# Kernel tuning notes

Measured on AMD Instinct MI355X. Metric: run time of the kernel, lower is better.

## Reference

```python
import jax, jax.numpy as jnp
from jax import lax
import numpy as np

B, C, HS, WS = 64, 1024, 23, 23  # backbone features (stride-16 of a 368x368 crop)
K = 28  # keypoints


def setup_inputs() -> dict:
    key = jax.random.key(0)
    ks = jax.random.split(key, 20)
    w = lambda k, shape, s=0.05: jax.random.normal(k, shape, jnp.float32) * s
    inp = {}
    inp["x"] = jax.random.normal(ks[0], (B, C, HS, WS), jnp.float32)
    # Residual(1024, 1024) block res5a (conv4 skipped: numIn == numOut, resConv False)
    inp["r5a_w1"] = w(ks[1], (512, 1024, 1, 1)); inp["r5a_b1"] = jnp.zeros(512, jnp.float32)
    inp["r5a_g1"] = jnp.ones(512, jnp.float32); inp["r5a_be1"] = jnp.zeros(512, jnp.float32)
    inp["r5a_m1"] = w(ks[2], (512,), 0.1)
    inp["r5a_v1"] = jax.random.uniform(ks[3], (512,), jnp.float32, 0.5, 1.5)
    inp["r5a_w2"] = w(ks[4], (512, 512, 3, 3)); inp["r5a_b2"] = jnp.zeros(512, jnp.float32)
    inp["r5a_g2"] = jnp.ones(512, jnp.float32); inp["r5a_be2"] = jnp.zeros(512, jnp.float32)
    inp["r5a_m2"] = w(ks[5], (512,), 0.1)
    inp["r5a_v2"] = jax.random.uniform(ks[6], (512,), jnp.float32, 0.5, 1.5)
    inp["r5a_w3"] = w(ks[7], (1024, 512, 1, 1)); inp["r5a_b3"] = jnp.zeros(1024, jnp.float32)
    # res5b 1x1 -> 3x3 -> 1x1
    inp["b1_w"] = w(ks[8], (256, 1024, 1, 1)); inp["b1_b"] = jnp.zeros(256, jnp.float32)
    inp["b2_w"] = w(ks[9], (128, 256, 3, 3)); inp["b2_b"] = jnp.zeros(128, jnp.float32)
    inp["b3_w"] = w(ks[10], (256, 128, 1, 1)); inp["b3_b"] = jnp.zeros(256, jnp.float32)
    # ConvTranspose2d weights kept in torch layout (Cin, Cout, kH, kW)
    inp["c1_w"] = w(ks[11], (256, 63, 4, 4)); inp["c1_b"] = jnp.zeros(63, jnp.float32)
    inp["c2_w"] = w(ks[12], (256, 128, 4, 4)); inp["c2_b"] = jnp.zeros(128, jnp.float32)
    # head convs
    inp["f1_w"] = w(ks[13], (128, 212, 3, 3)); inp["f1_b"] = jnp.zeros(128, jnp.float32)
    inp["f2_w"] = w(ks[14], (112, 128, 1, 1)); inp["f2_b"] = jnp.zeros(112, jnp.float32)
    return inp


_DN = ("NCHW", "OIHW", "NCHW")


def _conv(t, w, b, pad=0):
    y = lax.conv_general_dilated(t, w, (1, 1), [(pad, pad), (pad, pad)], dimension_numbers=_DN)
    return y + b[None, :, None, None]


def _deconv(t, w, b):
    # torch ConvTranspose2d(k=4, s=2, p=1): flip spatial, swap I/O, use lhs dilation
    wt = jnp.flip(w, (2, 3)).transpose(1, 0, 2, 3)  # (Cout, Cin, 4, 4)
    y = lax.conv_general_dilated(t, wt, (1, 1), [(2, 2), (2, 2)], lhs_dilation=(2, 2),
                                 dimension_numbers=_DN)
    return y + b[None, :, None, None]


def _bn(t, g, be, m, v):
    scale = g * lax.rsqrt(v + 1e-5)
    return (t - m[None, :, None, None]) * scale[None, :, None, None] + be[None, :, None, None]


def reference(x, r5a_w1, r5a_b1, r5a_g1, r5a_be1, r5a_m1, r5a_v1,
              r5a_w2, r5a_b2, r5a_g2, r5a_be2, r5a_m2, r5a_v2,
              r5a_w3, r5a_b3, b1_w, b1_b, b2_w, b2_b, b3_w, b3_b,
              c1_w, c1_b, c2_w, c2_b, f1_w, f1_b, f2_w, f2_b):
    # res5a: Residual(1024, 1024) -- identity shortcut (conv4 branch not taken)
    h = jax.nn.relu(_bn(_conv(x, r5a_w1, r5a_b1), r5a_g1, r5a_be1, r5a_m1, r5a_v1))
    h = jax.nn.relu(_bn(_conv(h, r5a_w2, r5a_b2, pad=1), r5a_g2, r5a_be2, r5a_m2, r5a_v2))
    h = _conv(h, r5a_w3, r5a_b3) + x
    # res5b
    h = _conv(h, b1_w, b1_b)
    h = _conv(h, b2_w, b2_b, pad=1)
    h = _conv(h, b3_w, b3_b)
    out1 = _deconv(h, c1_w, c1_b)              # [B, 63, 2H, 2W] location maps
    out2 = jax.nn.relu(_deconv(h, c2_w, c2_b))  # [B, 128, 2H, 2W]
    # per-keypoint location-map magnitude: sqrt(x^2 + y^2 + z^2) over interleaved channels
    out3 = jnp.sqrt(out1[:, ::3] ** 2 + out1[:, 1::3] ** 2 + out1[:, 2::3] ** 2)  # [B, 21, ...]
    cat = jnp.concatenate([out1, out2, out3], axis=1)  # 63 + 128 + 21 = 212 channels
    h = jax.nn.relu(_conv(cat, f1_w, f1_b, pad=1))
    h = _conv(h, f2_w, f2_b)                   # [B, 112, Hh, Wh]
    Bn, _, Hh, Wh = h.shape
    o = h.reshape(Bn, 4, Wh, Hh, K)            # faithful to torch .view(B, 4, W, H, 28)
    heatmap, map_x, map_y, map_z = o[:, 0], o[:, 1], o[:, 2], o[:, 3]
    hm_val = heatmap.max(axis=1)               # [B, Hh, K]
    hm_idx = heatmap.argmax(axis=1)            # [B, Hh, K]
    hm_idx2 = hm_val.argmax(axis=1)            # [B, K]
    hm_idx1 = jnp.take_along_axis(hm_idx, hm_idx2[:, None, :], axis=1)[:, 0]  # [B, K]
    bi = jnp.arange(Bn)[:, None]
    ki = jnp.arange(K)[None, :]
    vx = map_x[bi, hm_idx1, hm_idx2, ki]       # vectorized form of the nested python loop
    vy = map_y[bi, hm_idx1, hm_idx2, ki]
    vz = map_z[bi, hm_idx1, hm_idx2, ki]
    out_mod = jnp.stack([vx, vy, vz], axis=-1).reshape(Bn, 3 * K)  # [B, 84]
    return out_mod
```

## Files before the change

kernel.cpp:

```cpp
#include <hip/hip_runtime.h>
#include <math.h>

typedef __attribute__((ext_vector_type(8))) _Float16 f16x8;
typedef __attribute__((ext_vector_type(4))) float f32x4;

union HU { _Float16 h; unsigned short u; };

__device__ __forceinline__ void split32(float v, unsigned short& hh, unsigned short& ll) {
    HU a, b;
    a.h = (_Float16)v;
    b.h = (_Float16)(v - (float)a.h);
    hh = a.u; ll = b.u;
}
__device__ __forceinline__ float h2f(unsigned short s) { HU a; a.u = s; return (float)a.h; }

__device__ __forceinline__ void gload16(const unsigned short* g, unsigned short* l) {
    __builtin_amdgcn_global_load_lds(
        (const __attribute__((address_space(1))) unsigned int*)g,
        (__attribute__((address_space(3))) unsigned int*)l, 16, 0, 0);
}

struct ConvP {
    const unsigned short* in;
    const unsigned short* wr;
    const float* bias;
    const float* resx;
    unsigned short* out;
    long long loIn, loW, loOut;
    int H, W;
    int inWP, inPix0, inImg;
    int CIp, T, wRow, pxTotal;
    int oImg, oPix0, oYstr, oXstr, oC, oChOff, CO;
    int resCstr, resImg, relu;
    int shift[16];
    int woff[16];
};

template<int NFRAG>
__global__ __launch_bounds__(256) void convmm(ConvP p)
{
    __shared__ unsigned short lAh[128 * 32];
    __shared__ unsigned short lAl[128 * 32];
    __shared__ unsigned short lBh[128 * 32];
    __shared__ unsigned short lBl[128 * 32];

    const int tid  = threadIdx.x;
    const int w    = tid >> 6;
    const int lane = tid & 63;
    const int lo   = lane & 15, hi = lane >> 4;
    const int wm   = w >> 1,    wn = w & 1;
    const int HW   = p.H * p.W;

    long long aOff[2];
    const int aoct = lane & 3;
    for (int j = 0; j < 2; ++j) {
        int instr = 2 * w + j;
        int px = blockIdx.x * 128 + instr * 16 + (lane >> 2);
        if (px >= p.pxTotal) px = p.pxTotal - 1;
        int n = px / HW, pr = px - n * HW;
        int y = pr / p.W, x = pr - y * p.W;
        aOff[j] = ((long long)n * p.inImg + p.inPix0 + y * p.inWP + x) * (long long)p.CIp
                  + aoct * 8;
    }
    constexpr int NB = NFRAG / 2;
    long long bOff[NB];
    const int cob = blockIdx.y * (NFRAG * 32);
    for (int j = 0; j < NB; ++j) {
        int instr = NB * w + j;
        int col = instr * 16 + (lane >> 2);
        bOff[j] = (long long)(cob + col) * p.wRow + aoct * 8;
    }

    f32x4 acc[4][NFRAG];
#pragma unroll
    for (int q = 0; q < 4; ++q)
#pragma unroll
        for (int r = 0; r < NFRAG; ++r) acc[q][r] = (f32x4){0.f, 0.f, 0.f, 0.f};

    for (int t = 0; t < p.T; ++t) {
        const long long tShift = (long long)p.shift[t] * p.CIp;
        const int wo = p.woff[t];
        for (int ci0 = 0; ci0 < p.CIp; ci0 += 32) {
            __syncthreads();
#pragma unroll
            for (int j = 0; j < 2; ++j) {
                gload16(p.in + aOff[j] + tShift + ci0,          &lAh[(2 * w + j) * 512]);
                gload16(p.in + p.loIn + aOff[j] + tShift + ci0, &lAl[(2 * w + j) * 512]);
            }
#pragma unroll
            for (int j = 0; j < NB; ++j) {
                gload16(p.wr + bOff[j] + wo + ci0,         &lBh[(NB * w + j) * 512]);
                gload16(p.wr + p.loW + bOff[j] + wo + ci0, &lBl[(NB * w + j) * 512]);
            }
            __syncthreads();

            f16x8 aFh[4], aFl[4], bFh[NFRAG], bFl[NFRAG];
#pragma unroll
            for (int q = 0; q < 4; ++q) {
                int idx = (wm * 64 + q * 16 + lo) * 32 + hi * 8;
                aFh[q] = *(const f16x8*)&lAh[idx];
                aFl[q] = *(const f16x8*)&lAl[idx];
            }
#pragma unroll
            for (int r = 0; r < NFRAG; ++r) {
                int idx = (wn * NFRAG * 16 + r * 16 + lo) * 32 + hi * 8;
                bFh[r] = *(const f16x8*)&lBh[idx];
                bFl[r] = *(const f16x8*)&lBl[idx];
            }
#pragma unroll
            for (int q = 0; q < 4; ++q)
#pragma unroll
                for (int r = 0; r < NFRAG; ++r)
                    acc[q][r] = __builtin_amdgcn_mfma_f32_16x16x32_f16(
                        aFh[q], bFh[r], acc[q][r], 0, 0, 0);
#pragma unroll
            for (int q = 0; q < 4; ++q)
#pragma unroll
                for (int r = 0; r < NFRAG; ++r)
                    acc[q][r] = __builtin_amdgcn_mfma_f32_16x16x32_f16(
                        aFh[q], bFl[r], acc[q][r], 0, 0, 0);
#pragma unroll
            for (int q = 0; q < 4; ++q)
#pragma unroll
                for (int r = 0; r < NFRAG; ++r)
                    acc[q][r] = __builtin_amdgcn_mfma_f32_16x16x32_f16(
                        aFl[q], bFh[r], acc[q][r], 0, 0, 0);
        }
    }

    const int coB = cob + wn * NFRAG * 16;
#pragma unroll
    for (int q = 0; q < 4; ++q) {
        int pxBase = blockIdx.x * 128 + wm * 64 + q * 16 + hi * 4;
#pragma unroll
        for (int r4 = 0; r4 < 4; ++r4) {
            int px = pxBase + r4;
            if (px >= p.pxTotal) continue;
            int n = px / HW, pr = px - n * HW;
            int y = pr / p.W, x = pr - y * p.W;
            long long obase = ((long long)n * p.oImg + p.oPix0 + y * p.oYstr + x * p.oXstr)
                              * (long long)p.oC + p.oChOff;
#pragma unroll
            for (int nf = 0; nf < NFRAG; ++nf) {
                int co = coB + nf * 16 + lo;
                if (co < p.CO) {
                    float v = acc[q][nf][r4] + p.bias[co];
                    if (p.resx)
                        v += p.resx[(long long)n * p.resImg + (long long)co * p.resCstr + pr];
                    if (p.relu) v = fmaxf(v, 0.f);
                    unsigned short vh, vl;
                    split32(v, vh, vl);
                    p.out[obase + co] = vh;
                    p.out[p.loOut + obase + co] = vl;
                }
            }
        }
    }
}

__global__ __launch_bounds__(256) void prep_x(const float* __restrict__ in,
                                              unsigned short* __restrict__ xp,
                                              long long loOff)
{
    __shared__ float t[64][65];
    const int n = blockIdx.z, c0 = blockIdx.y * 64, px0 = blockIdx.x * 64;
    const int tid = threadIdx.x;
    const int colA = tid & 63, rowA = tid >> 6;
#pragma unroll
    for (int i = 0; i < 16; ++i) {
        int cl = i * 4 + rowA;
        int px = px0 + colA;
        float v = 0.f;
        if (px < 529) v = in[((size_t)n * 1024 + c0 + cl) * 529 + px];
        t[cl][colA] = v;
    }
    __syncthreads();
#pragma unroll
    for (int i = 0; i < 16; ++i) {
        int pxl = i * 4 + rowA;
        int px = px0 + pxl;
        if (px < 529) {
            unsigned short vh, vl;
            split32(t[colA][pxl], vh, vl);
            long long o = ((long long)n * 529 + px) * 1024 + c0 + colA;
            xp[o] = vh; xp[o + loOff] = vl;
        }
    }
}

__global__ __launch_bounds__(256) void prep_w(const float* __restrict__ src,
                                              unsigned short* __restrict__ dst, long long loW,
                                              int CO, int CI, int T, int COp, int CIp,
                                              const float* __restrict__ scale)
{
    long long idx = (long long)blockIdx.x * 256 + threadIdx.x;
    long long tot = (long long)COp * T * CIp;
    if (idx >= tot) return;
    int ci = idx % CIp; long long r = idx / CIp;
    int t = r % T; int co = r / T;
    float v = 0.f;
    if (co < CO && ci < CI) {
        v = src[((long long)co * CI + ci) * T + t];
        if (scale) v *= scale[co];
    }
    unsigned short vh, vl;
    split32(v, vh, vl);
    dst[idx] = vh; dst[idx + loW] = vl;
}

__global__ __launch_bounds__(256) void prep_w_deconv(const float* __restrict__ src,
                                                     unsigned short* __restrict__ dst,
                                                     long long loW, int CO)
{
    int idx = blockIdx.x * 256 + threadIdx.x;
    if (idx >= 128 * 16 * 256) return;
    int ci = idx & 255; int r = idx >> 8;
    int tap = r & 15; int co = r >> 4;
    int ky = tap >> 2, kx = tap & 3;
    float v = 0.f;
    if (co < CO) v = src[((size_t)ci * CO + co) * 16 + (3 - ky) * 4 + (3 - kx)];
    unsigned short vh, vl;
    split32(v, vh, vl);
    dst[idx] = vh; dst[idx + loW] = vl;
}

__global__ __launch_bounds__(512) void prep_sb(
    const float* g1, const float* be1, const float* m1, const float* v1, const float* b1,
    const float* g2, const float* be2, const float* m2, const float* v2, const float* b2,
    float* s1, float* bb1, float* s2, float* bb2)
{
    int i = threadIdx.x;
    float s = g1[i] * rsqrtf(v1[i] + 1e-5f);
    s1[i] = s; bb1[i] = (b1[i] - m1[i]) * s + be1[i];
    s = g2[i] * rsqrtf(v2[i] + 1e-5f);
    s2[i] = s; bb2[i] = (b2[i] - m2[i]) * s + be2[i];
}

__global__ __launch_bounds__(256) void zero_border(unsigned short* buf,
                                                   int HP, int WP, int C, int nb)
{
    long long idx = (long long)blockIdx.x * 256 + threadIdx.x;
    long long tot = (long long)64 * nb * C;
    if (idx >= tot) return;
    int c = idx % C; long long r = idx / C;
    int b = r % nb; int n = r / nb;
    int pp;
    if (b < WP) pp = b;
    else if (b < 2 * WP) pp = (HP - 1) * WP + (b - WP);
    else { int q = b - 2 * WP; int row = 1 + (q >> 1); pp = row * WP + ((q & 1) ? (WP - 1) : 0); }
    buf[((long long)n * HP * WP + pp) * C + c] = 0;
}

__global__ __launch_bounds__(256) void zero_chpad(unsigned short* cat)
{
    long long idx = (long long)blockIdx.x * 256 + threadIdx.x;
    if (idx >= (long long)64 * 2304 * 12) return;
    int c = 212 + (int)(idx % 12);
    long long pp = idx / 12;
    cat[pp * 224 + c] = 0;
}

__global__ __launch_bounds__(256) void out3_k(unsigned short* cat, long long loOff)
{
    long long idx = (long long)blockIdx.x * 256 + threadIdx.x;
    if (idx >= (long long)64 * 2116 * 21) return;
    int j = idx % 21; long long r = idx / 21;
    int pr = r % 2116; int n = r / 2116;
    int y = pr / 46, x = pr - y * 46;
    long long base = ((long long)n * 2304 + (y + 1) * 48 + (x + 1)) * 224;
    float a = h2f(cat[base + 3 * j])     + h2f(cat[base + 3 * j + loOff]);
    float b = h2f(cat[base + 3 * j + 1]) + h2f(cat[base + 3 * j + 1 + loOff]);
    float c = h2f(cat[base + 3 * j + 2]) + h2f(cat[base + 3 * j + 2 + loOff]);
    unsigned short vh, vl;
    split32(sqrtf(a * a + b * b + c * c), vh, vl);
    cat[base + 191 + j] = vh;
    cat[base + 191 + j + loOff] = vl;
}

__global__ __launch_bounds__(64) void argmax_hl(const unsigned short* __restrict__ h,
                                                long long loOff, float* __restrict__ outp)
{
    const int k = blockIdx.x, n = blockIdx.y, t = threadIdx.x;
    const unsigned short* b = h + (size_t)n * 2116 * 112;
    float best = -INFINITY; int ba = 0; int bb = t;
    if (t < 46) {
        for (int a = 0; a < 46; ++a) {
            int f = a * 1288 + t * 28 + k;
            int c = f / 2116, pr = f - c * 2116;
            long long e = (long long)pr * 112 + c;
            float v = h2f(b[e]) + h2f(b[e + loOff]);
            if (v > best) { best = v; ba = a; }
        }
    }
#pragma unroll
    for (int off = 32; off > 0; off >>= 1) {
        float ov = __shfl_down(best, off);
        int oa = __shfl_down(ba, off), ob = __shfl_down(bb, off);
        if (ov > best || (ov == best && ob < bb)) { best = ov; ba = oa; bb = ob; }
    }
    if (t == 0) {
        for (int q = 1; q <= 3; ++q) {
            int f = q * 59248 + ba * 1288 + bb * 28 + k;
            int c = f / 2116, pr = f - c * 2116;
            long long e = (long long)pr * 112 + c;
            outp[(size_t)n * 84 + k * 3 + (q - 1)] = h2f(b[e]) + h2f(b[e + loOff]);
        }
    }
}

extern "C" void kernel_launch(void* const* d_in, const int* in_sizes, int n_in,
                              void* d_out, int out_size, void* d_ws, size_t ws_size,
                              hipStream_t stream)
{
    const float* x   = (const float*)d_in[0];
    const float* w1  = (const float*)d_in[1];
    const float* rb1 = (const float*)d_in[2];
    const float* g1  = (const float*)d_in[3];
    const float* be1 = (const float*)d_in[4];
    const float* m1  = (const float*)d_in[5];
    const float* v1  = (const float*)d_in[6];
    const float* w2  = (const float*)d_in[7];
    const float* rb2 = (const float*)d_in[8];
    const float* g2  = (const float*)d_in[9];
    const float* be2 = (const float*)d_in[10];
    const float* m2  = (const float*)d_in[11];
    const float* v2  = (const float*)d_in[12];
    const float* w3  = (const float*)d_in[13];
    const float* rb3 = (const float*)d_in[14];
    const float* b1w = (const float*)d_in[15];
    const float* b1b = (const float*)d_in[16];
    const float* b2w = (const float*)d_in[17];
    const float* b2b = (const float*)d_in[18];
    const float* b3w = (const float*)d_in[19];
    const float* b3b = (const float*)d_in[20];
    const float* c1w = (const float*)d_in[21];
    const float* c1b = (const float*)d_in[22];
    const float* c2w = (const float*)d_in[23];
    const float* c2b = (const float*)d_in[24];
    const float* f1w = (const float*)d_in[25];
    const float* f1b = (const float*)d_in[26];
    const float* f2w = (const float*)d_in[27];
    const float* f2b = (const float*)d_in[28];

    unsigned short* wsb = (unsigned short*)d_ws;
    size_t woffE = 0;
    auto walloc = [&](size_t planeElems) {
        unsigned short* p = wsb + woffE; woffE += 2 * planeElems; return p;
    };
    unsigned short* Wr1  = walloc(524288);
    unsigned short* Wr2  = walloc(2359296);
    unsigned short* Wr3  = walloc(524288);
    unsigned short* Wr4  = walloc(262144);
    unsigned short* Wr5  = walloc(294912);
    unsigned short* Wr6  = walloc(32768);
    unsigned short* Wr7  = walloc(524288);
    unsigned short* Wr8  = walloc(524288);
    unsigned short* Wr9  = walloc(258048);
    unsigned short* Wr10 = walloc(16384);
    char* fscr = (char*)d_ws + 23068672;
    float* s1  = (float*)(fscr);
    float* bb1 = (float*)(fscr + 2048);
    float* s2  = (float*)(fscr + 4096);
    float* bb2 = (float*)(fscr + 6144);

    unsigned short* XPU = wsb + 12582912;
    unsigned short* R1  = wsb + 81920000;
    unsigned short* R2  = wsb + 12582912;
    unsigned short* R3  = wsb + 47251456;
    unsigned short* B1  = wsb + 116588544;
    unsigned short* B2  = wsb + 12582912;
    unsigned short* B3  = wsb + 21250048;
    unsigned short* CAT = wsb + 47251456;
    unsigned short* F1  = wsb + 12582912;
    unsigned short* F2  = wsb + 47251456;
    const long long XPU_L = 34668544, R1_L = 20480000, R2_L = 17334272, R3_L = 34668544;
    const long long B1_L = 10240000, B2_L = 4333568, B3_L = 10240000;
    const long long CAT_L = 33030144, F1_L = 17334272, F2_L = 15167488;

    prep_sb<<<1, 512, 0, stream>>>(g1, be1, m1, v1, rb1, g2, be2, m2, v2, rb2, s1, bb1, s2, bb2);
    auto pw = [&](const float* src, unsigned short* dst, long long loW, int CO, int CI,
                  int T, int COp, int CIp, const float* sc) {
        long long tot = (long long)COp * T * CIp;
        prep_w<<<(tot + 255) / 256, 256, 0, stream>>>(src, dst, loW, CO, CI, T, COp, CIp, sc);
    };
    pw(w1,  Wr1, 524288,  512, 1024, 1, 512, 1024, s1);
    pw(w2,  Wr2, 2359296, 512, 512,  9, 512, 512,  s2);
    pw(w3,  Wr3, 524288,  1024, 512, 1, 1024, 512, nullptr);
    pw(b1w, Wr4, 262144,  256, 1024, 1, 256, 1024, nullptr);
    pw(b2w, Wr5, 294912,  128, 256,  9, 128, 256,  nullptr);
    pw(b3w, Wr6, 32768,   256, 128,  1, 256, 128,  nullptr);
    prep_w_deconv<<<(128 * 16 * 256) / 256, 256, 0, stream>>>(c1w, Wr7, 524288, 63);
    prep_w_deconv<<<(128 * 16 * 256) / 256, 256, 0, stream>>>(c2w, Wr8, 524288, 128);
    pw(f1w, Wr9, 258048,  128, 212,  9, 128, 224,  nullptr);
    pw(f2w, Wr10, 16384,  112, 128,  1, 128, 128,  nullptr);
    prep_x<<<dim3(9, 16, 64), 256, 0, stream>>>(x, XPU, XPU_L);

    auto zb = [&](unsigned short* buf, long long loOff, int HP, int WP, int C) {
        int nb = 2 * WP + 2 * (HP - 2);
        long long tot = (long long)64 * nb * C;
        zero_border<<<(tot + 255) / 256, 256, 0, stream>>>(buf, HP, WP, C, nb);
        zero_border<<<(tot + 255) / 256, 256, 0, stream>>>(buf + loOff, HP, WP, C, nb);
    };

    auto conv = [&](int NFRAG, const unsigned short* in, long long loIn,
                    const unsigned short* wr, long long loW,
                    const float* bias, const float* resx, unsigned short* outp, long long loOut,
                    int H, int W, int inWP, int inPix0, int inImg, int CIp, int T, int wRow,
                    int oImg, int oPix0, int oYstr, int oXstr, int oC, int oChOff, int CO,
                    int relu, const int* shifts, const int* woffs) {
        ConvP p{};
        p.in = in; p.wr = wr; p.bias = bias; p.resx = resx; p.out = outp;
        p.loIn = loIn; p.loW = loW; p.loOut = loOut;
        p.H = H; p.W = W; p.inWP = inWP; p.inPix0 = inPix0; p.inImg = inImg;
        p.CIp = CIp; p.T = T; p.wRow = wRow; p.pxTotal = 64 * H * W;
        p.oImg = oImg; p.oPix0 = oPix0; p.oYstr = oYstr; p.oXstr = oXstr;
        p.oC = oC; p.oChOff = oChOff; p.CO = CO;
        p.resCstr = 529; p.resImg = 541696; p.relu = relu;
        for (int t = 0; t < T; ++t) { p.shift[t] = shifts[t]; p.woff[t] = woffs[t]; }
        int BN = NFRAG * 32;
        dim3 grid((p.pxTotal + 127) / 128, (CO + BN - 1) / BN);
        if (NFRAG == 4) convmm<4><<<grid, 256, 0, stream>>>(p);
        else            convmm<2><<<grid, 256, 0, stream>>>(p);
    };

    int z16[16] = {0};
    int sh9_25[16], wo9_512[16], wo9_256[16], sh9_48[16], wo9_224[16];
    for (int t = 0; t < 9; ++t) {
        int ky = t / 3, kx = t % 3;
        sh9_25[t] = (ky - 1) * 25 + (kx - 1);
        sh9_48[t] = (ky - 1) * 48 + (kx - 1);
        wo9_512[t] = t * 512; wo9_256[t] = t * 256; wo9_224[t] = t * 224;
    }

    zb(R1, R1_L, 25, 25, 512);
    conv(4, XPU, XPU_L, Wr1, 524288, bb1, nullptr, R1, R1_L,
         23, 23, 23, 0, 529, 1024, 1, 1024, 625, 26, 25, 1, 512, 0, 512, 1, z16, z16);
    conv(4, R1, R1_L, Wr2, 2359296, bb2, nullptr, R2, R2_L,
         23, 23, 25, 26, 625, 512, 9, 9 * 512, 529, 0, 23, 1, 512, 0, 512, 1, sh9_25, wo9_512);
    zb(B1, B1_L, 25, 25, 256);
    conv(4, R2, R2_L, Wr3, 524288, rb3, x, R3, R3_L,
         23, 23, 23, 0, 529, 512, 1, 512, 529, 0, 23, 1, 1024, 0, 1024, 0, z16, z16);
    zb(B3, B3_L, 25, 25, 256);
    conv(4, R3, R3_L, Wr4, 262144, b1b, nullptr, B1, B1_L,
         23, 23, 23, 0, 529, 1024, 1, 1024, 625, 26, 25, 1, 256, 0, 256, 0, z16, z16);
    zb(CAT, CAT_L, 48, 48, 224);
    {
        long long tot = (long long)64 * 2304 * 12;
        zero_chpad<<<(tot + 255) / 256, 256, 0, stream>>>(CAT);
        zero_chpad<<<(tot + 255) / 256, 256, 0, stream>>>(CAT + CAT_L);
    }
    conv(4, B1, B1_L, Wr5, 294912, b2b, nullptr, B2, B2_L,
         23, 23, 25, 26, 625, 256, 9, 9 * 256, 529, 0, 23, 1, 128, 0, 128, 0, sh9_25, wo9_256);
    conv(4, B2, B2_L, Wr6, 32768, b3b, nullptr, B3, B3_L,
         23, 23, 23, 0, 529, 128, 1, 128, 625, 26, 25, 1, 256, 0, 256, 0, z16, z16);

    for (int a = 0; a < 2; ++a)
        for (int b = 0; b < 2; ++b) {
            int sh[16], wo[16];
            for (int ty = 0; ty < 2; ++ty)
                for (int tx = 0; tx < 2; ++tx) {
                    int tI = ty * 2 + tx;
                    sh[tI] = (a + ty - 1) * 25 + (b + tx - 1);
                    wo[tI] = ((a + 2 * ty) * 4 + (b + 2 * tx)) * 256;
                }
            int oPix0 = (a + 1) * 48 + (b + 1);
            conv(2, B3, B3_L, Wr7, 524288, c1b, nullptr, CAT, CAT_L,
                 23, 23, 25, 26, 625, 256, 4, 16 * 256, 2304, oPix0, 96, 2, 224, 0, 63,
                 0, sh, wo);
            conv(4, B3, B3_L, Wr8, 524288, c2b, nullptr, CAT, CAT_L,
                 23, 23, 25, 26, 625, 256, 4, 16 * 256, 2304, oPix0, 96, 2, 224, 63, 128,
                 1, sh, wo);
        }
    {
        long long tot = (long long)64 * 2116 * 21;
        out3_k<<<(tot + 255) / 256, 256, 0, stream>>>(CAT, CAT_L);
    }

    conv(4, CAT, CAT_L, Wr9, 258048, f1b, nullptr, F1, F1_L,
         46, 46, 48, 49, 2304, 224, 9, 9 * 224, 2116, 0, 46, 1, 128, 0, 128, 1,
         sh9_48, wo9_224);
    conv(2, F1, F1_L, Wr10, 16384, f2b, nullptr, F2, F2_L,
         46, 46, 46, 0, 2116, 128, 1, 128, 2116, 0, 46, 1, 112, 0, 112, 0, z16, z16);

    argmax_hl<<<dim3(28, 64), dim3(64), 0, stream>>>(F2, F2_L, (float*)d_out);
}
```

Baseline: 2.559 ms.

## Stage halo input tile once per channel chunk for spatial convolutions

Adds a convhalo kernel that loads a contiguous input window, covering the 128-pixel block plus its halo, into LDS once per 32-channel chunk. All taps then read from it through shifted offsets, and only the weight tiles are double-buffered per tap. The goal is to stop re-fetching the input tile for every one of the 9 (or 4) taps, cutting global and LDS traffic for the 3x3 convs and the deconv phases. It also remaps workgroups across the 8 XCDs so neighbouring blocks share cache, and it groups images into units. In exchange it uses a larger LDS footprint and adds a sync per tap, and the halo indexing must stay within the padded buffers.

```diff
diff --git a/kernel.cpp b/kernel.cpp
--- a/kernel.cpp
+++ b/kernel.cpp
@@ -147,6 +147,169 @@
                     float v = acc[q][nf][r4] + p.bias[co];
                     if (p.resx)
                         v += p.resx[(long long)n * p.resImg + (long long)co * p.resCstr + pr];
+                    if (p.relu) v = fmaxf(v, 0.f);
+                    unsigned short vh, vl;
+                    split32(v, vh, vl);
+                    p.out[obase + co] = vh;
+                    p.out[p.loOut + obase + co] = vl;
+                }
+            }
+        }
+    }
+}
+
+struct HConvP {
+    const unsigned short* in;
+    const unsigned short* wr;
+    const float* bias;
+    unsigned short* out;
+    long long loIn, loW, loOut;
+    int W, IMG_PX, UNIT, UNIT_PX, BPI, nUnits;
+    int inWP, inPix0, inImg, halo;
+    int CIp, T, wRow;
+    int oImg, oPix0, oYstr, oXstr, oC, oChOff, CO;
+    int relu;
+    int shift[16];
+    int woff[16];
+};
+
+template<int NFRAG>
+__global__ __launch_bounds__(256) void convhalo(HConvP p)
+{
+    __shared__ unsigned short sA[2 * 8192];
+    __shared__ unsigned short sB[2][8192];
+
+    const int tid  = threadIdx.x;
+    const int w    = tid >> 6;
+    const int lane = tid & 63;
+    const int lo   = lane & 15, hi = lane >> 4;
+    const int hi8  = hi * 8;
+    const int wm   = w >> 1,    wn = w & 1;
+
+    const int nwg = gridDim.x, orig = blockIdx.x;
+    const int q8 = nwg >> 3, r8 = nwg & 7;
+    const int xcd = orig & 7, lcl = orig >> 3;
+    const int l = (xcd < r8 ? xcd * (q8 + 1) : r8 * (q8 + 1) + (xcd - r8) * q8) + lcl;
+    const int upb = p.nUnits * p.BPI;
+    const int co_blk = l / upb;
+    const int rest = l - co_blk * upb;
+    const int unit = rest / p.BPI;
+    const int b = rest - unit * p.BPI;
+    const int cob = co_blk * (NFRAG * 32);
+
+    const int px0 = b * 128;
+    const int n0 = unit * p.UNIT + px0 / p.IMG_PX;
+    const int pr0 = px0 % p.IMG_PX;
+    const long long stageBase = (long long)n0 * p.inImg + p.inPix0
+                                + (pr0 / p.W) * p.inWP + (pr0 % p.W) - p.halo;
+
+    int lpx[4];
+#pragma unroll
+    for (int q = 0; q < 4; ++q) {
+        int pl = px0 + wm * 64 + q * 16 + lo;
+        if (pl >= p.UNIT_PX) pl = p.UNIT_PX - 1;
+        int nn = unit * p.UNIT + pl / p.IMG_PX;
+        int pr = pl % p.IMG_PX;
+        long long pp = (long long)nn * p.inImg + p.inPix0
+                       + (pr / p.W) * p.inWP + (pr % p.W);
+        lpx[q] = (int)(pp - stageBase);
+    }
+
+    const unsigned short* srcA = p.in + (stageBase + (lane >> 2)) * (long long)p.CIp
+                                 + (lane & 3) * 8;
+
+    auto stageA = [&](int ci0) {
+#pragma unroll
+        for (int j = w; j < 16; j += 4) {
+            long long o = (long long)j * 16 * p.CIp + ci0;
+            gload16(srcA + o,          &sA[j * 512]);
+            gload16(srcA + o + p.loIn, &sA[8192 + j * 512]);
+        }
+    };
+    auto stageB = [&](int buf, int t, int ci0) {
+        long long wb = (long long)p.woff[t] + ci0 + (lane & 3) * 8;
+#pragma unroll
+        for (int j = w; j < 2 * NFRAG; j += 4) {
+            long long o = (long long)(cob + j * 16 + (lane >> 2)) * p.wRow + wb;
+            gload16(p.wr + o,         &sB[buf][j * 512]);
+            gload16(p.wr + o + p.loW, &sB[buf][4096 + j * 512]);
+        }
+    };
+
+    f32x4 acc[4][NFRAG];
+#pragma unroll
+    for (int q = 0; q < 4; ++q)
+#pragma unroll
+        for (int r = 0; r < NFRAG; ++r) acc[q][r] = (f32x4){0.f, 0.f, 0.f, 0.f};
+
+    stageA(0);
+    stageB(0, 0, 0);
+    __syncthreads();
+    int cur = 0;
+
+    for (int ci0 = 0;;) {
+        for (int t = 0; t < p.T; ++t) {
+            const int sh = p.shift[t];
+            f16x8 aFh[4], aFl[4], bFh[NFRAG], bFl[NFRAG];
+#pragma unroll
+            for (int q = 0; q < 4; ++q) {
+                int e = (lpx[q] + sh) * 32 + hi8;
+                aFh[q] = *(const f16x8*)&sA[e];
+                aFl[q] = *(const f16x8*)&sA[8192 + e];
+            }
+#pragma unroll
+            for (int r = 0; r < NFRAG; ++r) {
+                int e = (wn * NFRAG * 16 + r * 16 + lo) * 32 + hi8;
+                bFh[r] = *(const f16x8*)&sB[cur][e];
+                bFl[r] = *(const f16x8*)&sB[cur][4096 + e];
+            }
+            if (t + 1 < p.T) stageB(cur ^ 1, t + 1, ci0);
+#pragma unroll
+            for (int q = 0; q < 4; ++q)
+#pragma unroll
+                for (int r = 0; r < NFRAG; ++r)
+                    acc[q][r] = __builtin_amdgcn_mfma_f32_16x16x32_f16(
+                        aFh[q], bFh[r], acc[q][r], 0, 0, 0);
+#pragma unroll
+            for (int q = 0; q < 4; ++q)
+#pragma unroll
+                for (int r = 0; r < NFRAG; ++r)
+                    acc[q][r] = __builtin_amdgcn_mfma_f32_16x16x32_f16(
+                        aFh[q], bFl[r], acc[q][r], 0, 0, 0);
+#pragma unroll
+            for (int q = 0; q < 4; ++q)
+#pragma unroll
+                for (int r = 0; r < NFRAG; ++r)
+                    acc[q][r] = __builtin_amdgcn_mfma_f32_16x16x32_f16(
+                        aFl[q], bFh[r], acc[q][r], 0, 0, 0);
+            if (t + 1 < p.T) { __syncthreads(); cur ^= 1; }
+        }
+        ci0 += 32;
+        if (ci0 >= p.CIp) break;
+        __syncthreads();
+        stageA(ci0);
+        stageB(cur ^ 1, 0, ci0);
+        __syncthreads();
+        cur ^= 1;
+    }
+
+    const int coB = cob + wn * NFRAG * 16;
+#pragma unroll
+    for (int q = 0; q < 4; ++q) {
+#pragma unroll
+        for (int r4 = 0; r4 < 4; ++r4) {
+            int pl = px0 + wm * 64 + q * 16 + hi * 4 + r4;
+            if (pl >= p.UNIT_PX) continue;
+            int nn = unit * p.UNIT + pl / p.IMG_PX;
+            int pr = pl % p.IMG_PX;
+            int y = pr / p.W, x = pr - y * p.W;
+            long long obase = ((long long)nn * p.oImg + p.oPix0 + y * p.oYstr + x * p.oXstr)
+                              * (long long)p.oC + p.oChOff;
+#pragma unroll
+            for (int nf = 0; nf < NFRAG; ++nf) {
+                int co = coB + nf * 16 + lo;
+                if (co < p.CO) {
+                    float v = acc[q][nf][r4] + p.bias[co];
                     if (p.relu) v = fmaxf(v, 0.f);
                     unsigned short vh, vl;
                     split32(v, vh, vl);
@@ -423,6 +586,31 @@
         else            convmm<2><<<grid, 256, 0, stream>>>(p);
     };
 
+    auto hconv = [&](int NFRAG, const unsigned short* in, long long loIn,
+                     const unsigned short* wr, long long loW, const float* bias,
+                     unsigned short* outp, long long loOut,
+                     int W, int IMG_PX, int UNIT, int UNIT_PX, int BPI,
+                     int inWP, int inPix0, int inImg,
+                     int CIp, int T, int wRow,
+                     int oImg, int oPix0, int oYstr, int oXstr, int oC, int oChOff, int CO,
+                     int relu, const int* shifts, const int* woffs) {
+        HConvP p{};
+        p.in = in; p.wr = wr; p.bias = bias; p.out = outp;
+        p.loIn = loIn; p.loW = loW; p.loOut = loOut;
+        p.W = W; p.IMG_PX = IMG_PX; p.UNIT = UNIT; p.UNIT_PX = UNIT_PX; p.BPI = BPI;
+        p.nUnits = 64 / UNIT;
+        p.inWP = inWP; p.inPix0 = inPix0; p.inImg = inImg; p.halo = inWP + 1;
+        p.CIp = CIp; p.T = T; p.wRow = wRow;
+        p.oImg = oImg; p.oPix0 = oPix0; p.oYstr = oYstr; p.oXstr = oXstr;
+        p.oC = oC; p.oChOff = oChOff; p.CO = CO; p.relu = relu;
+        for (int t = 0; t < T; ++t) { p.shift[t] = shifts[t]; p.woff[t] = woffs[t]; }
+        int BN = NFRAG * 32;
+        int nCo = (CO + BN - 1) / BN;
+        dim3 grid(nCo * p.nUnits * BPI);
+        if (NFRAG == 4) convhalo<4><<<grid, 256, 0, stream>>>(p);
+        else            convhalo<2><<<grid, 256, 0, stream>>>(p);
+    };
+
     int z16[16] = {0};
     int sh9_25[16], wo9_512[16], wo9_256[16], sh9_48[16], wo9_224[16];
     for (int t = 0; t < 9; ++t) {
@@ -435,8 +623,9 @@
     zb(R1, R1_L, 25, 25, 512);
     conv(4, XPU, XPU_L, Wr1, 524288, bb1, nullptr, R1, R1_L,
          23, 23, 23, 0, 529, 1024, 1, 1024, 625, 26, 25, 1, 512, 0, 512, 1, z16, z16);
-    conv(4, R1, R1_L, Wr2, 2359296, bb2, nullptr, R2, R2_L,
-         23, 23, 25, 26, 625, 512, 9, 9 * 512, 529, 0, 23, 1, 512, 0, 512, 1, sh9_25, wo9_512);
+    hconv(4, R1, R1_L, Wr2, 2359296, bb2, R2, R2_L,
+          23, 529, 2, 1058, 9, 25, 26, 625, 512, 9, 9 * 512,
+          529, 0, 23, 1, 512, 0, 512, 1, sh9_25, wo9_512);
     zb(B1, B1_L, 25, 25, 256);
     conv(4, R2, R2_L, Wr3, 524288, rb3, x, R3, R3_L,
          23, 23, 23, 0, 529, 512, 1, 512, 529, 0, 23, 1, 1024, 0, 1024, 0, z16, z16);
@@ -449,8 +638,9 @@
         zero_chpad<<<(tot + 255) / 256, 256, 0, stream>>>(CAT);
         zero_chpad<<<(tot + 255) / 256, 256, 0, stream>>>(CAT + CAT_L);
     }
-    conv(4, B1, B1_L, Wr5, 294912, b2b, nullptr, B2, B2_L,
-         23, 23, 25, 26, 625, 256, 9, 9 * 256, 529, 0, 23, 1, 128, 0, 128, 0, sh9_25, wo9_256);
+    hconv(4, B1, B1_L, Wr5, 294912, b2b, B2, B2_L,
+          23, 529, 2, 1058, 9, 25, 26, 625, 256, 9, 9 * 256,
+          529, 0, 23, 1, 128, 0, 128, 0, sh9_25, wo9_256);
     conv(4, B2, B2_L, Wr6, 32768, b3b, nullptr, B3, B3_L,
          23, 23, 23, 0, 529, 128, 1, 128, 625, 26, 25, 1, 256, 0, 256, 0, z16, z16);
 
@@ -464,21 +654,21 @@
                     wo[tI] = ((a + 2 * ty) * 4 + (b + 2 * tx)) * 256;
                 }
             int oPix0 = (a + 1) * 48 + (b + 1);
-            conv(2, B3, B3_L, Wr7, 524288, c1b, nullptr, CAT, CAT_L,
-                 23, 23, 25, 26, 625, 256, 4, 16 * 256, 2304, oPix0, 96, 2, 224, 0, 63,
-                 0, sh, wo);
-            conv(4, B3, B3_L, Wr8, 524288, c2b, nullptr, CAT, CAT_L,
-                 23, 23, 25, 26, 625, 256, 4, 16 * 256, 2304, oPix0, 96, 2, 224, 63, 128,
-                 1, sh, wo);
+            hconv(2, B3, B3_L, Wr7, 524288, c1b, CAT, CAT_L,
+                  23, 529, 2, 1058, 9, 25, 26, 625, 256, 4, 16 * 256,
+                  2304, oPix0, 96, 2, 224, 0, 63, 0, sh, wo);
+            hconv(4, B3, B3_L, Wr8, 524288, c2b, CAT, CAT_L,
+                  23, 529, 2, 1058, 9, 25, 26, 625, 256, 4, 16 * 256,
+                  2304, oPix0, 96, 2, 224, 63, 128, 1, sh, wo);
         }
     {
         long long tot = (long long)64 * 2116 * 21;
         out3_k<<<(tot + 255) / 256, 256, 0, stream>>>(CAT, CAT_L);
     }
 
-    conv(4, CAT, CAT_L, Wr9, 258048, f1b, nullptr, F1, F1_L,
-         46, 46, 48, 49, 2304, 224, 9, 9 * 224, 2116, 0, 46, 1, 128, 0, 128, 1,
-         sh9_48, wo9_224);
+    hconv(4, CAT, CAT_L, Wr9, 258048, f1b, F1, F1_L,
+          46, 2116, 1, 2116, 17, 48, 49, 2304, 224, 9, 9 * 224,
+          2116, 0, 46, 1, 128, 0, 128, 1, sh9_48, wo9_224);
     conv(2, F1, F1_L, Wr10, 16384, f2b, nullptr, F2, F2_L,
          46, 46, 46, 0, 2116, 128, 1, 128, 2116, 0, 46, 1, 112, 0, 112, 0, z16, z16);
 
```

Result: faster. 2.350 ms (-8.2%).
